# Kernel tuning notes

Hardware: AMD Instinct MI355X
Metric: run time of the kernel (lower is better)

## Reference

```python
import jax, jax.numpy as jnp
import numpy as np

FLOOR = 1e-12
B, C, T = 64, 80, 8000


def setup_inputs() -> dict:
    key = jax.random.key(0)
    k1, k2 = jax.random.split(key)
    x = jax.random.uniform(k1, (B, C, T), dtype=jnp.float32)  # nonneg energies
    x_length = jax.random.randint(k2, (B,), 1, T + 1, dtype=jnp.int32)
    # learned PCEN parameters (init values from module defaults)
    alpha = jnp.full((C,), 0.96, dtype=jnp.float32)
    delta = jnp.full((C,), 2.0, dtype=jnp.float32)
    root = jnp.full((C,), 2.0, dtype=jnp.float32)
    ema_w = jnp.full((C,), 0.04, dtype=jnp.float32)  # per-channel smooth coef (sPCEN)
    return {"x": x, "alpha": alpha, "delta": delta, "root": root,
            "ema_w": ema_w, "x_length": x_length}


def _ema(x, w):
    """Exponential moving average along time. x: (B,C,T), w: (C,). acc init = x[:,:,0]."""
    xt = jnp.moveaxis(x, 2, 0)  # (T, B, C)

    def step(acc, xi):
        acc = w * xi + (1.0 - w) * acc
        return acc, acc

    _, ys = jax.lax.scan(step, x[:, :, 0], xt)  # ys: (T, B, C)
    return jnp.moveaxis(ys, 0, 2)  # (B, C, T)


def reference(x, alpha, delta, root, ema_w, x_length):
    w = jnp.clip(ema_w, 0.0, 1.0)
    a = jnp.minimum(alpha, 1.0)[None, :, None]
    r = jnp.maximum(root, 1.0)[None, :, None]
    d = delta[None, :, None]
    m = _ema(x, w)  # (B, C, T)
    one_over_root = 1.0 / r
    out = (x / (FLOOR + m) ** a + d) ** one_over_root - d ** one_over_root
    return (out, x_length)
```

## Files before the change

kernel.cpp:

```cpp
#include <hip/hip_runtime.h>
#include <cmath>


constexpr int T_LEN = 8000;
constexpr int T4    = T_LEN / 4;
constexpr int BLK   = 256;
constexpr int NTILE = (T4 + BLK - 1) / BLK;

__device__ __forceinline__ float fexp2(float x) { return __builtin_amdgcn_exp2f(x); }
__device__ __forceinline__ float flog2(float x) { return __builtin_amdgcn_logf(x); }
__device__ __forceinline__ float fsqrt(float x) { return __builtin_amdgcn_sqrtf(x); }

__global__ __launch_bounds__(BLK, 8) void pcen_kernel(
    const float* __restrict__ x, const float* __restrict__ alpha,
    const float* __restrict__ delta, const float* __restrict__ root,
    const float* __restrict__ ema_w, const int* __restrict__ xlen,
    float* __restrict__ out, int C, int rows, int nlen)
{
    __shared__ float wB[2][4];

    const int tid  = threadIdx.x;
    const int lane = tid & 63;
    const int wid  = tid >> 6;
    const int row  = blockIdx.x;
    const int c    = row % C;

    const float w     = fminf(fmaxf(ema_w[c], 0.0f), 1.0f);
    const float p     = 1.0f - w;
    const float na    = -fminf(alpha[c], 1.0f);
    const float r     = fmaxf(root[c], 1.0f);
    const float inv_r = 1.0f / r;
    const float d     = delta[c];
    const bool  use_sqrt = (r == 2.0f);
    const float droot = use_sqrt ? fsqrt(d) : fexp2(inv_r * flog2(d));

    const float p4 = p * p * p * p;
    const float c1 = p4, c2 = c1 * c1, c3 = c2 * c2,
                c4 = c3 * c3, c5 = c4 * c4, c6 = c5 * c5;
    const float q  = c6 * c6;
    const float q2 = q * q, q3 = q2 * q, q4 = q2 * q2;
    const float lp  = flog2(p);
    const float p4l = (lane == 0) ? 1.0f : fexp2(4.0f * (float)lane * lp);
    const float qw  = (wid == 0) ? 1.0f : (wid == 1) ? q : (wid == 2) ? q2 : q3;

    const float4* x4 = reinterpret_cast<const float4*>(x + (size_t)row * T_LEN);
    float4*       o4 = reinterpret_cast<float4*>(out + (size_t)row * T_LEN);

    float carry = x[(size_t)row * T_LEN];

    float4 v = (tid < T4) ? x4[tid] : make_float4(0.f, 0.f, 0.f, 0.f);

    for (int t = 0; t < NTILE; ++t) {
        const int  j      = t * BLK + tid;
        const bool active = (j < T4);
        const int  par    = t & 1;

        float s = v.x;
        s = fmaf(s, p, v.y); s = fmaf(s, p, v.z); s = fmaf(s, p, v.w);
        float b = active ? (w * s) : 0.0f;

        float pb;
        pb = __shfl_up(b,  1, 64); if (lane >=  1) b = fmaf(c1, pb, b);
        pb = __shfl_up(b,  2, 64); if (lane >=  2) b = fmaf(c2, pb, b);
        pb = __shfl_up(b,  4, 64); if (lane >=  4) b = fmaf(c3, pb, b);
        pb = __shfl_up(b,  8, 64); if (lane >=  8) b = fmaf(c4, pb, b);
        pb = __shfl_up(b, 16, 64); if (lane >= 16) b = fmaf(c5, pb, b);
        pb = __shfl_up(b, 32, 64); if (lane >= 32) b = fmaf(c6, pb, b);

        if (lane == 63) wB[par][wid] = b;
        float eb = __shfl_up(b, 1, 64);
        if (lane == 0) eb = 0.0f;
        __syncthreads();

        float4 vn = make_float4(0.f, 0.f, 0.f, 0.f);
        const int jn = j + BLK;
        if (jn < T4) vn = x4[jn];

        const float W0 = wB[par][0], W1 = wB[par][1], W2 = wB[par][2], W3 = wB[par][3];
        float Pb = 0.0f;
        if (wid == 1) Pb = W0;
        else if (wid == 2) Pb = fmaf(q, W0, W1);
        else if (wid == 3) Pb = fmaf(q, fmaf(q, W0, W1), W2);
        const float base = fmaf(qw, carry, Pb);
        float acc = fmaf(p4l, base, eb);

        const float Tb = fmaf(q, fmaf(q, fmaf(q, W0, W1), W2), W3);
        carry = fmaf(q4, carry, Tb);

        if (active) {
            float4 u = v, o;
            if (use_sqrt) {
                acc = fmaf(w, u.x, p * acc);
                o.x = fsqrt(fmaf(u.x, fexp2(na * flog2(acc + 1e-12f)), d)) - droot;
                acc = fmaf(w, u.y, p * acc);
                o.y = fsqrt(fmaf(u.y, fexp2(na * flog2(acc + 1e-12f)), d)) - droot;
                acc = fmaf(w, u.z, p * acc);
                o.z = fsqrt(fmaf(u.z, fexp2(na * flog2(acc + 1e-12f)), d)) - droot;
                acc = fmaf(w, u.w, p * acc);
                o.w = fsqrt(fmaf(u.w, fexp2(na * flog2(acc + 1e-12f)), d)) - droot;
            } else {
                acc = fmaf(w, u.x, p * acc);
                o.x = fexp2(inv_r * flog2(fmaf(u.x, fexp2(na * flog2(acc + 1e-12f)), d))) - droot;
                acc = fmaf(w, u.y, p * acc);
                o.y = fexp2(inv_r * flog2(fmaf(u.y, fexp2(na * flog2(acc + 1e-12f)), d))) - droot;
                acc = fmaf(w, u.z, p * acc);
                o.z = fexp2(inv_r * flog2(fmaf(u.z, fexp2(na * flog2(acc + 1e-12f)), d))) - droot;
                acc = fmaf(w, u.w, p * acc);
                o.w = fexp2(inv_r * flog2(fmaf(u.w, fexp2(na * flog2(acc + 1e-12f)), d))) - droot;
            }
            o4[j] = o;
        }
        v = vn;
    }

    if (row == 0) {
        for (int i = tid; i < nlen; i += BLK)
            out[(size_t)rows * T_LEN + i] = (float)xlen[i];
    }
}

extern "C" void kernel_launch(void* const* d_in, const int* in_sizes, int n_in,
                              void* d_out, int out_size, void* d_ws, size_t ws_size,
                              hipStream_t stream) {
    const float* x     = (const float*)d_in[0];
    const float* alpha = (const float*)d_in[1];
    const float* delta = (const float*)d_in[2];
    const float* root  = (const float*)d_in[3];
    const float* emaw  = (const float*)d_in[4];
    const int*   xlen  = (const int*)d_in[5];
    float*       out   = (float*)d_out;

    const int C    = in_sizes[1];
    const int rows = in_sizes[0] / T_LEN;
    const int nlen = in_sizes[5];

    hipLaunchKernelGGL(pcen_kernel, dim3(rows), dim3(BLK), 0, stream,
                       x, alpha, delta, root, emaw, xlen, out, C, rows, nlen);
}
```

Measured before the change: 65.84 us.

## Assign one wavefront per row to eliminate block-level barrier in EMA scan

Each 64-lane wavefront now processes a whole row on its own, so the cross-wave combine through shared memory and the __syncthreads per tile are gone. The carry between tiles is passed with a lane-63 broadcast shuffle. The cost is a serial loop per wave that is four times longer (32 tiles instead of 8) with less memory-level parallelism per row. The grid shrinks to 1280 blocks, which lowers per-block overhead.

```diff
diff --git a/kernel.cpp b/kernel.cpp
--- a/kernel.cpp
+++ b/kernel.cpp
@@ -5,7 +5,7 @@
 constexpr int T_LEN = 8000;
 constexpr int T4    = T_LEN / 4;
 constexpr int BLK   = 256;
-constexpr int NTILE = (T4 + BLK - 1) / BLK;
+constexpr int NT    = (T4 + 63) / 64;
 
 __device__ __forceinline__ float fexp2(float x) { return __builtin_amdgcn_exp2f(x); }
 __device__ __forceinline__ float flog2(float x) { return __builtin_amdgcn_logf(x); }
@@ -17,104 +17,92 @@
     const float* __restrict__ ema_w, const int* __restrict__ xlen,
     float* __restrict__ out, int C, int rows, int nlen)
 {
-    __shared__ float wB[2][4];
-
     const int tid  = threadIdx.x;
     const int lane = tid & 63;
     const int wid  = tid >> 6;
-    const int row  = blockIdx.x;
-    const int c    = row % C;
+    const int row  = blockIdx.x * 4 + wid;
 
-    const float w     = fminf(fmaxf(ema_w[c], 0.0f), 1.0f);
-    const float p     = 1.0f - w;
-    const float na    = -fminf(alpha[c], 1.0f);
-    const float r     = fmaxf(root[c], 1.0f);
-    const float inv_r = 1.0f / r;
-    const float d     = delta[c];
-    const bool  use_sqrt = (r == 2.0f);
-    const float droot = use_sqrt ? fsqrt(d) : fexp2(inv_r * flog2(d));
+    if (row < rows) {
+        const int c = row % C;
 
-    const float p4 = p * p * p * p;
-    const float c1 = p4, c2 = c1 * c1, c3 = c2 * c2,
-                c4 = c3 * c3, c5 = c4 * c4, c6 = c5 * c5;
-    const float q  = c6 * c6;
-    const float q2 = q * q, q3 = q2 * q, q4 = q2 * q2;
-    const float lp  = flog2(p);
-    const float p4l = (lane == 0) ? 1.0f : fexp2(4.0f * (float)lane * lp);
-    const float qw  = (wid == 0) ? 1.0f : (wid == 1) ? q : (wid == 2) ? q2 : q3;
+        const float w     = fminf(fmaxf(ema_w[c], 0.0f), 1.0f);
+        const float p     = 1.0f - w;
+        const float na    = -fminf(alpha[c], 1.0f);
+        const float r     = fmaxf(root[c], 1.0f);
+        const float inv_r = 1.0f / r;
+        const float d     = delta[c];
+        const bool  use_sqrt = (r == 2.0f);
+        const float droot = use_sqrt ? fsqrt(d) : fexp2(inv_r * flog2(d));
 
-    const float4* x4 = reinterpret_cast<const float4*>(x + (size_t)row * T_LEN);
-    float4*       o4 = reinterpret_cast<float4*>(out + (size_t)row * T_LEN);
+        const float c1 = p * p * p * p;
+        const float c2 = c1 * c1, c3 = c2 * c2, c4 = c3 * c3,
+                    c5 = c4 * c4, c6 = c5 * c5;
+        const float q  = c6 * c6;
+        const float lp  = flog2(p);
+        const float p4l = (lane == 0) ? 1.0f : fexp2(4.0f * (float)lane * lp);
 
-    float carry = x[(size_t)row * T_LEN];
+        const float4* x4 = reinterpret_cast<const float4*>(x + (size_t)row * T_LEN);
+        float4*       o4 = reinterpret_cast<float4*>(out + (size_t)row * T_LEN);
 
-    float4 v = (tid < T4) ? x4[tid] : make_float4(0.f, 0.f, 0.f, 0.f);
+        float4 v = x4[lane];
+        float carry = __shfl(v.x, 0, 64);
 
-    for (int t = 0; t < NTILE; ++t) {
-        const int  j      = t * BLK + tid;
-        const bool active = (j < T4);
-        const int  par    = t & 1;
+        for (int t = 0; t < NT; ++t) {
+            const int  j      = t * 64 + lane;
+            const bool active = (j < T4);
 
-        float s = v.x;
-        s = fmaf(s, p, v.y); s = fmaf(s, p, v.z); s = fmaf(s, p, v.w);
-        float b = active ? (w * s) : 0.0f;
+            const int jn = j + 64;
+            float4 vn = make_float4(0.f, 0.f, 0.f, 0.f);
+            if (jn < T4) vn = x4[jn];
 
-        float pb;
-        pb = __shfl_up(b,  1, 64); if (lane >=  1) b = fmaf(c1, pb, b);
-        pb = __shfl_up(b,  2, 64); if (lane >=  2) b = fmaf(c2, pb, b);
-        pb = __shfl_up(b,  4, 64); if (lane >=  4) b = fmaf(c3, pb, b);
-        pb = __shfl_up(b,  8, 64); if (lane >=  8) b = fmaf(c4, pb, b);
-        pb = __shfl_up(b, 16, 64); if (lane >= 16) b = fmaf(c5, pb, b);
-        pb = __shfl_up(b, 32, 64); if (lane >= 32) b = fmaf(c6, pb, b);
+            float s = v.x;
+            s = fmaf(s, p, v.y); s = fmaf(s, p, v.z); s = fmaf(s, p, v.w);
+            float b = active ? (w * s) : 0.0f;
 
-        if (lane == 63) wB[par][wid] = b;
-        float eb = __shfl_up(b, 1, 64);
-        if (lane == 0) eb = 0.0f;
-        __syncthreads();
+            float pb;
+            pb = __shfl_up(b,  1, 64); if (lane >=  1) b = fmaf(c1, pb, b);
+            pb = __shfl_up(b,  2, 64); if (lane >=  2) b = fmaf(c2, pb, b);
+            pb = __shfl_up(b,  4, 64); if (lane >=  4) b = fmaf(c3, pb, b);
+            pb = __shfl_up(b,  8, 64); if (lane >=  8) b = fmaf(c4, pb, b);
+            pb = __shfl_up(b, 16, 64); if (lane >= 16) b = fmaf(c5, pb, b);
+            pb = __shfl_up(b, 32, 64); if (lane >= 32) b = fmaf(c6, pb, b);
 
-        float4 vn = make_float4(0.f, 0.f, 0.f, 0.f);
-        const int jn = j + BLK;
-        if (jn < T4) vn = x4[jn];
+            float eb = __shfl_up(b, 1, 64);
+            if (lane == 0) eb = 0.0f;
+            const float tb = __shfl(b, 63, 64);
 
-        const float W0 = wB[par][0], W1 = wB[par][1], W2 = wB[par][2], W3 = wB[par][3];
-        float Pb = 0.0f;
-        if (wid == 1) Pb = W0;
-        else if (wid == 2) Pb = fmaf(q, W0, W1);
-        else if (wid == 3) Pb = fmaf(q, fmaf(q, W0, W1), W2);
-        const float base = fmaf(qw, carry, Pb);
-        float acc = fmaf(p4l, base, eb);
+            float acc = fmaf(p4l, carry, eb);
+            carry = fmaf(q, carry, tb);
 
-        const float Tb = fmaf(q, fmaf(q, fmaf(q, W0, W1), W2), W3);
-        carry = fmaf(q4, carry, Tb);
-
-        if (active) {
-            float4 u = v, o;
-            if (use_sqrt) {
-                acc = fmaf(w, u.x, p * acc);
-                o.x = fsqrt(fmaf(u.x, fexp2(na * flog2(acc + 1e-12f)), d)) - droot;
-                acc = fmaf(w, u.y, p * acc);
-                o.y = fsqrt(fmaf(u.y, fexp2(na * flog2(acc + 1e-12f)), d)) - droot;
-                acc = fmaf(w, u.z, p * acc);
-                o.z = fsqrt(fmaf(u.z, fexp2(na * flog2(acc + 1e-12f)), d)) - droot;
-                acc = fmaf(w, u.w, p * acc);
-                o.w = fsqrt(fmaf(u.w, fexp2(na * flog2(acc + 1e-12f)), d)) - droot;
-            } else {
-                acc = fmaf(w, u.x, p * acc);
-                o.x = fexp2(inv_r * flog2(fmaf(u.x, fexp2(na * flog2(acc + 1e-12f)), d))) - droot;
-                acc = fmaf(w, u.y, p * acc);
-                o.y = fexp2(inv_r * flog2(fmaf(u.y, fexp2(na * flog2(acc + 1e-12f)), d))) - droot;
-                acc = fmaf(w, u.z, p * acc);
-                o.z = fexp2(inv_r * flog2(fmaf(u.z, fexp2(na * flog2(acc + 1e-12f)), d))) - droot;
-                acc = fmaf(w, u.w, p * acc);
-                o.w = fexp2(inv_r * flog2(fmaf(u.w, fexp2(na * flog2(acc + 1e-12f)), d))) - droot;
+            if (active) {
+                float4 u = v, o;
+                if (use_sqrt) {
+                    acc = fmaf(w, u.x, p * acc);
+                    o.x = fsqrt(fmaf(u.x, fexp2(na * flog2(acc + 1e-12f)), d)) - droot;
+                    acc = fmaf(w, u.y, p * acc);
+                    o.y = fsqrt(fmaf(u.y, fexp2(na * flog2(acc + 1e-12f)), d)) - droot;
+                    acc = fmaf(w, u.z, p * acc);
+                    o.z = fsqrt(fmaf(u.z, fexp2(na * flog2(acc + 1e-12f)), d)) - droot;
+                    acc = fmaf(w, u.w, p * acc);
+                    o.w = fsqrt(fmaf(u.w, fexp2(na * flog2(acc + 1e-12f)), d)) - droot;
+                } else {
+                    acc = fmaf(w, u.x, p * acc);
+                    o.x = fexp2(inv_r * flog2(fmaf(u.x, fexp2(na * flog2(acc + 1e-12f)), d))) - droot;
+                    acc = fmaf(w, u.y, p * acc);
+                    o.y = fexp2(inv_r * flog2(fmaf(u.y, fexp2(na * flog2(acc + 1e-12f)), d))) - droot;
+                    acc = fmaf(w, u.z, p * acc);
+                    o.z = fexp2(inv_r * flog2(fmaf(u.z, fexp2(na * flog2(acc + 1e-12f)), d))) - droot;
+                    acc = fmaf(w, u.w, p * acc);
+                    o.w = fexp2(inv_r * flog2(fmaf(u.w, fexp2(na * flog2(acc + 1e-12f)), d))) - droot;
+                }
+                o4[j] = o;
             }
-            o4[j] = o;
+            v = vn;
         }
-        v = vn;
     }
 
-    if (row == 0) {
-        for (int i = tid; i < nlen; i += BLK)
+    if (blockIdx.x == 0 && wid == 0) {
+        for (int i = lane; i < nlen; i += 64)
             out[(size_t)rows * T_LEN + i] = (float)xlen[i];
     }
 }
@@ -134,6 +122,7 @@
     const int rows = in_sizes[0] / T_LEN;
     const int nlen = in_sizes[5];
 
-    hipLaunchKernelGGL(pcen_kernel, dim3(rows), dim3(BLK), 0, stream,
+    const int nblk = (rows + 3) / 4;
+    hipLaunchKernelGGL(pcen_kernel, dim3(nblk), dim3(BLK), 0, stream,
                        x, alpha, delta, root, emaw, xlen, out, C, rows, nlen);
 }
```

Result: slower. 70.99 us (+7.8%).

## Process two float4 chunks per thread per tile to halve block barriers

Applied to the files above, without the earlier changes.

Each tile now covers 512 float4 (two per thread), so the scan runs interleaved low/high wave scans and chains two carries per tile. This cuts the number of __syncthreads and serial tile iterations per row from 8 to 4, and the next tile's loads are now issued before the scan rather than after the barrier. In exchange it uses more registers, so launch bounds drop from 8 to 6 waves-per-EU hints, which may lower occupancy.

```diff
diff --git a/kernel.cpp b/kernel.cpp
--- a/kernel.cpp
+++ b/kernel.cpp
@@ -5,19 +5,20 @@
 constexpr int T_LEN = 8000;
 constexpr int T4    = T_LEN / 4;
 constexpr int BLK   = 256;
-constexpr int NTILE = (T4 + BLK - 1) / BLK;
+constexpr int TILE4 = BLK * 2;
+constexpr int NTILE = (T4 + TILE4 - 1) / TILE4;
 
 __device__ __forceinline__ float fexp2(float x) { return __builtin_amdgcn_exp2f(x); }
 __device__ __forceinline__ float flog2(float x) { return __builtin_amdgcn_logf(x); }
 __device__ __forceinline__ float fsqrt(float x) { return __builtin_amdgcn_sqrtf(x); }
 
-__global__ __launch_bounds__(BLK, 8) void pcen_kernel(
+__global__ __launch_bounds__(BLK, 6) void pcen_kernel(
     const float* __restrict__ x, const float* __restrict__ alpha,
     const float* __restrict__ delta, const float* __restrict__ root,
     const float* __restrict__ ema_w, const int* __restrict__ xlen,
     float* __restrict__ out, int C, int rows, int nlen)
 {
-    __shared__ float wB[2][4];
+    __shared__ float wLo[2][4], wHi[2][4];
 
     const int tid  = threadIdx.x;
     const int lane = tid & 63;
@@ -34,11 +35,12 @@
     const bool  use_sqrt = (r == 2.0f);
     const float droot = use_sqrt ? fsqrt(d) : fexp2(inv_r * flog2(d));
 
-    const float p4 = p * p * p * p;
-    const float c1 = p4, c2 = c1 * c1, c3 = c2 * c2,
-                c4 = c3 * c3, c5 = c4 * c4, c6 = c5 * c5;
+    const float c1 = p * p * p * p;
+    const float c2 = c1 * c1, c3 = c2 * c2, c4 = c3 * c3,
+                c5 = c4 * c4, c6 = c5 * c5;
     const float q  = c6 * c6;
-    const float q2 = q * q, q3 = q2 * q, q4 = q2 * q2;
+    const float q2 = q * q, q3 = q2 * q;
+    const float ql = q2 * q2;
     const float lp  = flog2(p);
     const float p4l = (lane == 0) ? 1.0f : fexp2(4.0f * (float)lane * lp);
     const float qw  = (wid == 0) ? 1.0f : (wid == 1) ? q : (wid == 2) ? q2 : q3;
@@ -48,69 +50,117 @@
 
     float carry = x[(size_t)row * T_LEN];
 
-    float4 v = (tid < T4) ? x4[tid] : make_float4(0.f, 0.f, 0.f, 0.f);
+    float4 v0 = x4[tid];
+    float4 v1 = x4[tid + BLK];
 
     for (int t = 0; t < NTILE; ++t) {
-        const int  j      = t * BLK + tid;
-        const bool active = (j < T4);
+        const int  j0     = t * TILE4 + tid;
+        const int  j1     = j0 + BLK;
+        const bool hi_act = (j1 < T4);
         const int  par    = t & 1;
 
-        float s = v.x;
-        s = fmaf(s, p, v.y); s = fmaf(s, p, v.z); s = fmaf(s, p, v.w);
-        float b = active ? (w * s) : 0.0f;
+        float4 n0 = make_float4(0.f, 0.f, 0.f, 0.f);
+        float4 n1 = make_float4(0.f, 0.f, 0.f, 0.f);
+        const int k0 = j0 + TILE4, k1 = j1 + TILE4;
+        if (t + 1 < NTILE) {
+            n0 = x4[k0];
+            if (k1 < T4) n1 = x4[k1];
+        }
 
-        float pb;
-        pb = __shfl_up(b,  1, 64); if (lane >=  1) b = fmaf(c1, pb, b);
-        pb = __shfl_up(b,  2, 64); if (lane >=  2) b = fmaf(c2, pb, b);
-        pb = __shfl_up(b,  4, 64); if (lane >=  4) b = fmaf(c3, pb, b);
-        pb = __shfl_up(b,  8, 64); if (lane >=  8) b = fmaf(c4, pb, b);
-        pb = __shfl_up(b, 16, 64); if (lane >= 16) b = fmaf(c5, pb, b);
-        pb = __shfl_up(b, 32, 64); if (lane >= 32) b = fmaf(c6, pb, b);
+        float sl = v0.x;
+        sl = fmaf(sl, p, v0.y); sl = fmaf(sl, p, v0.z); sl = fmaf(sl, p, v0.w);
+        float bl = w * sl;
+        float sh = v1.x;
+        sh = fmaf(sh, p, v1.y); sh = fmaf(sh, p, v1.z); sh = fmaf(sh, p, v1.w);
+        float bh = hi_act ? (w * sh) : 0.0f;
 
-        if (lane == 63) wB[par][wid] = b;
-        float eb = __shfl_up(b, 1, 64);
-        if (lane == 0) eb = 0.0f;
+        float pl, ph;
+        pl = __shfl_up(bl,  1, 64); ph = __shfl_up(bh,  1, 64);
+        if (lane >=  1) { bl = fmaf(c1, pl, bl); bh = fmaf(c1, ph, bh); }
+        pl = __shfl_up(bl,  2, 64); ph = __shfl_up(bh,  2, 64);
+        if (lane >=  2) { bl = fmaf(c2, pl, bl); bh = fmaf(c2, ph, bh); }
+        pl = __shfl_up(bl,  4, 64); ph = __shfl_up(bh,  4, 64);
+        if (lane >=  4) { bl = fmaf(c3, pl, bl); bh = fmaf(c3, ph, bh); }
+        pl = __shfl_up(bl,  8, 64); ph = __shfl_up(bh,  8, 64);
+        if (lane >=  8) { bl = fmaf(c4, pl, bl); bh = fmaf(c4, ph, bh); }
+        pl = __shfl_up(bl, 16, 64); ph = __shfl_up(bh, 16, 64);
+        if (lane >= 16) { bl = fmaf(c5, pl, bl); bh = fmaf(c5, ph, bh); }
+        pl = __shfl_up(bl, 32, 64); ph = __shfl_up(bh, 32, 64);
+        if (lane >= 32) { bl = fmaf(c6, pl, bl); bh = fmaf(c6, ph, bh); }
+
+        if (lane == 63) { wLo[par][wid] = bl; wHi[par][wid] = bh; }
+        float ebl = __shfl_up(bl, 1, 64);
+        float ebh = __shfl_up(bh, 1, 64);
+        if (lane == 0) { ebl = 0.0f; ebh = 0.0f; }
         __syncthreads();
 
-        float4 vn = make_float4(0.f, 0.f, 0.f, 0.f);
-        const int jn = j + BLK;
-        if (jn < T4) vn = x4[jn];
+        const float L0 = wLo[par][0], L1 = wLo[par][1], L2 = wLo[par][2], L3 = wLo[par][3];
+        const float H0 = wHi[par][0], H1 = wHi[par][1], H2 = wHi[par][2], H3 = wHi[par][3];
+        float PL = 0.0f, PH = 0.0f;
+        if (wid == 1)      { PL = L0;                        PH = H0; }
+        else if (wid == 2) { PL = fmaf(q, L0, L1);           PH = fmaf(q, H0, H1); }
+        else if (wid == 3) { PL = fmaf(q, fmaf(q, L0, L1), L2);
+                             PH = fmaf(q, fmaf(q, H0, H1), H2); }
+        const float TloB = fmaf(q, fmaf(q, fmaf(q, L0, L1), L2), L3);
+        const float ThiB = fmaf(q, fmaf(q, fmaf(q, H0, H1), H2), H3);
 
-        const float W0 = wB[par][0], W1 = wB[par][1], W2 = wB[par][2], W3 = wB[par][3];
-        float Pb = 0.0f;
-        if (wid == 1) Pb = W0;
-        else if (wid == 2) Pb = fmaf(q, W0, W1);
-        else if (wid == 3) Pb = fmaf(q, fmaf(q, W0, W1), W2);
-        const float base = fmaf(qw, carry, Pb);
-        float acc = fmaf(p4l, base, eb);
+        const float Elo = fmaf(qw, carry, PL);
+        const float mid = fmaf(ql, carry, TloB);
+        const float Ehi = fmaf(qw, mid, PH);
+        carry = fmaf(ql, mid, ThiB);
 
-        const float Tb = fmaf(q, fmaf(q, fmaf(q, W0, W1), W2), W3);
-        carry = fmaf(q4, carry, Tb);
+        float accl = fmaf(p4l, Elo, ebl);
+        float acch = fmaf(p4l, Ehi, ebh);
 
-        if (active) {
-            float4 u = v, o;
+        {
+            float4 u = v0, o;
             if (use_sqrt) {
-                acc = fmaf(w, u.x, p * acc);
-                o.x = fsqrt(fmaf(u.x, fexp2(na * flog2(acc + 1e-12f)), d)) - droot;
-                acc = fmaf(w, u.y, p * acc);
-                o.y = fsqrt(fmaf(u.y, fexp2(na * flog2(acc + 1e-12f)), d)) - droot;
-                acc = fmaf(w, u.z, p * acc);
-                o.z = fsqrt(fmaf(u.z, fexp2(na * flog2(acc + 1e-12f)), d)) - droot;
-                acc = fmaf(w, u.w, p * acc);
-                o.w = fsqrt(fmaf(u.w, fexp2(na * flog2(acc + 1e-12f)), d)) - droot;
+                accl = fmaf(w, u.x, p * accl);
+                o.x = fsqrt(fmaf(u.x, fexp2(na * flog2(accl + 1e-12f)), d)) - droot;
+                accl = fmaf(w, u.y, p * accl);
+                o.y = fsqrt(fmaf(u.y, fexp2(na * flog2(accl + 1e-12f)), d)) - droot;
+                accl = fmaf(w, u.z, p * accl);
+                o.z = fsqrt(fmaf(u.z, fexp2(na * flog2(accl + 1e-12f)), d)) - droot;
+                accl = fmaf(w, u.w, p * accl);
+                o.w = fsqrt(fmaf(u.w, fexp2(na * flog2(accl + 1e-12f)), d)) - droot;
             } else {
-                acc = fmaf(w, u.x, p * acc);
-                o.x = fexp2(inv_r * flog2(fmaf(u.x, fexp2(na * flog2(acc + 1e-12f)), d))) - droot;
-                acc = fmaf(w, u.y, p * acc);
-                o.y = fexp2(inv_r * flog2(fmaf(u.y, fexp2(na * flog2(acc + 1e-12f)), d))) - droot;
-                acc = fmaf(w, u.z, p * acc);
-                o.z = fexp2(inv_r * flog2(fmaf(u.z, fexp2(na * flog2(acc + 1e-12f)), d))) - droot;
-                acc = fmaf(w, u.w, p * acc);
-                o.w = fexp2(inv_r * flog2(fmaf(u.w, fexp2(na * flog2(acc + 1e-12f)), d))) - droot;
+                accl = fmaf(w, u.x, p * accl);
+                o.x = fexp2(inv_r * flog2(fmaf(u.x, fexp2(na * flog2(accl + 1e-12f)), d))) - droot;
+                accl = fmaf(w, u.y, p * accl);
+                o.y = fexp2(inv_r * flog2(fmaf(u.y, fexp2(na * flog2(accl + 1e-12f)), d))) - droot;
+                accl = fmaf(w, u.z, p * accl);
+                o.z = fexp2(inv_r * flog2(fmaf(u.z, fexp2(na * flog2(accl + 1e-12f)), d))) - droot;
+                accl = fmaf(w, u.w, p * accl);
+                o.w = fexp2(inv_r * flog2(fmaf(u.w, fexp2(na * flog2(accl + 1e-12f)), d))) - droot;
             }
-            o4[j] = o;
+            o4[j0] = o;
         }
-        v = vn;
+        if (hi_act) {
+            float4 u = v1, o;
+            if (use_sqrt) {
+                acch = fmaf(w, u.x, p * acch);
+                o.x = fsqrt(fmaf(u.x, fexp2(na * flog2(acch + 1e-12f)), d)) - droot;
+                acch = fmaf(w, u.y, p * acch);
+                o.y = fsqrt(fmaf(u.y, fexp2(na * flog2(acch + 1e-12f)), d)) - droot;
+                acch = fmaf(w, u.z, p * acch);
+                o.z = fsqrt(fmaf(u.z, fexp2(na * flog2(acch + 1e-12f)), d)) - droot;
+                acch = fmaf(w, u.w, p * acch);
+                o.w = fsqrt(fmaf(u.w, fexp2(na * flog2(acch + 1e-12f)), d)) - droot;
+            } else {
+                acch = fmaf(w, u.x, p * acch);
+                o.x = fexp2(inv_r * flog2(fmaf(u.x, fexp2(na * flog2(acch + 1e-12f)), d))) - droot;
+                acch = fmaf(w, u.y, p * acch);
+                o.y = fexp2(inv_r * flog2(fmaf(u.y, fexp2(na * flog2(acch + 1e-12f)), d))) - droot;
+                acch = fmaf(w, u.z, p * acch);
+                o.z = fexp2(inv_r * flog2(fmaf(u.z, fexp2(na * flog2(acch + 1e-12f)), d))) - droot;
+                acch = fmaf(w, u.w, p * acch);
+                o.w = fexp2(inv_r * flog2(fmaf(u.w, fexp2(na * flog2(acch + 1e-12f)), d))) - droot;
+            }
+            o4[j1] = o;
+        }
+
+        v0 = n0;
+        v1 = n1;
     }
 
     if (row == 0) {
```

Measured after the change: 64.71 us. Within noise of the previous version (-1.7%).

## Load whole row into registers and batch scans with single barrier

Applied to the files above, without the earlier changes.

Each block now loads all 8 float4 tiles of its row up front, runs the eight intra-wave shuffle scans interleaved, and syncs once instead of once per tile. The carry is then chained across tiles serially. Output uses nontemporal stores, and the launch-bounds occupancy hint drops from 8 to 6 to make room for the extra registers. This gives more loads in flight and more independent shuffles at the cost of higher register pressure and lower occupancy.

```diff
diff --git a/kernel.cpp b/kernel.cpp
--- a/kernel.cpp
+++ b/kernel.cpp
@@ -5,19 +5,26 @@
 constexpr int T_LEN = 8000;
 constexpr int T4    = T_LEN / 4;
 constexpr int BLK   = 256;
-constexpr int NTILE = (T4 + BLK - 1) / BLK;
+constexpr int NH    = 8;
+
+typedef float f32x4 __attribute__((ext_vector_type(4)));
 
 __device__ __forceinline__ float fexp2(float x) { return __builtin_amdgcn_exp2f(x); }
 __device__ __forceinline__ float flog2(float x) { return __builtin_amdgcn_logf(x); }
 __device__ __forceinline__ float fsqrt(float x) { return __builtin_amdgcn_sqrtf(x); }
 
-__global__ __launch_bounds__(BLK, 8) void pcen_kernel(
+__device__ __forceinline__ void nt_store4(float* dst, float a, float b, float c, float d) {
+    f32x4 v = { a, b, c, d };
+    __builtin_nontemporal_store(v, reinterpret_cast<f32x4*>(dst));
+}
+
+__global__ __launch_bounds__(BLK, 6) void pcen_kernel(
     const float* __restrict__ x, const float* __restrict__ alpha,
     const float* __restrict__ delta, const float* __restrict__ root,
     const float* __restrict__ ema_w, const int* __restrict__ xlen,
     float* __restrict__ out, int C, int rows, int nlen)
 {
-    __shared__ float wB[2][4];
+    __shared__ float wS[NH][4];
 
     const int tid  = threadIdx.x;
     const int lane = tid & 63;
@@ -34,83 +41,98 @@
     const bool  use_sqrt = (r == 2.0f);
     const float droot = use_sqrt ? fsqrt(d) : fexp2(inv_r * flog2(d));
 
-    const float p4 = p * p * p * p;
-    const float c1 = p4, c2 = c1 * c1, c3 = c2 * c2,
-                c4 = c3 * c3, c5 = c4 * c4, c6 = c5 * c5;
+    const float c1 = p * p * p * p;
+    const float c2 = c1 * c1, c3 = c2 * c2, c4 = c3 * c3,
+                c5 = c4 * c4, c6 = c5 * c5;
     const float q  = c6 * c6;
-    const float q2 = q * q, q3 = q2 * q, q4 = q2 * q2;
+    const float q2 = q * q, q3 = q2 * q;
+    const float ql = q2 * q2;
     const float lp  = flog2(p);
     const float p4l = (lane == 0) ? 1.0f : fexp2(4.0f * (float)lane * lp);
     const float qw  = (wid == 0) ? 1.0f : (wid == 1) ? q : (wid == 2) ? q2 : q3;
 
-    const float4* x4 = reinterpret_cast<const float4*>(x + (size_t)row * T_LEN);
-    float4*       o4 = reinterpret_cast<float4*>(out + (size_t)row * T_LEN);
+    const float4* x4   = reinterpret_cast<const float4*>(x + (size_t)row * T_LEN);
+    float*        orow = out + (size_t)row * T_LEN;
 
+    float4 v[NH];
+    #pragma unroll
+    for (int h = 0; h < NH; ++h) {
+        const int j = h * BLK + tid;
+        if (j < T4) v[h] = x4[j];
+        else        v[h] = make_float4(0.f, 0.f, 0.f, 0.f);
+    }
     float carry = x[(size_t)row * T_LEN];
 
-    float4 v = (tid < T4) ? x4[tid] : make_float4(0.f, 0.f, 0.f, 0.f);
+    float b[NH];
+    #pragma unroll
+    for (int h = 0; h < NH; ++h) {
+        float s = v[h].x;
+        s = fmaf(s, p, v[h].y); s = fmaf(s, p, v[h].z); s = fmaf(s, p, v[h].w);
+        b[h] = w * s;
+    }
 
-    for (int t = 0; t < NTILE; ++t) {
-        const int  j      = t * BLK + tid;
-        const bool active = (j < T4);
-        const int  par    = t & 1;
+    {
+        float pb;
+        #pragma unroll
+        for (int h = 0; h < NH; ++h) { pb = __shfl_up(b[h],  1, 64); if (lane >=  1) b[h] = fmaf(c1, pb, b[h]); }
+        #pragma unroll
+        for (int h = 0; h < NH; ++h) { pb = __shfl_up(b[h],  2, 64); if (lane >=  2) b[h] = fmaf(c2, pb, b[h]); }
+        #pragma unroll
+        for (int h = 0; h < NH; ++h) { pb = __shfl_up(b[h],  4, 64); if (lane >=  4) b[h] = fmaf(c3, pb, b[h]); }
+        #pragma unroll
+        for (int h = 0; h < NH; ++h) { pb = __shfl_up(b[h],  8, 64); if (lane >=  8) b[h] = fmaf(c4, pb, b[h]); }
+        #pragma unroll
+        for (int h = 0; h < NH; ++h) { pb = __shfl_up(b[h], 16, 64); if (lane >= 16) b[h] = fmaf(c5, pb, b[h]); }
+        #pragma unroll
+        for (int h = 0; h < NH; ++h) { pb = __shfl_up(b[h], 32, 64); if (lane >= 32) b[h] = fmaf(c6, pb, b[h]); }
+    }
 
-        float s = v.x;
-        s = fmaf(s, p, v.y); s = fmaf(s, p, v.z); s = fmaf(s, p, v.w);
-        float b = active ? (w * s) : 0.0f;
+    float eb[NH];
+    #pragma unroll
+    for (int h = 0; h < NH; ++h) {
+        if (lane == 63) wS[h][wid] = b[h];
+        eb[h] = __shfl_up(b[h], 1, 64);
+        if (lane == 0) eb[h] = 0.0f;
+    }
+    __syncthreads();
 
-        float pb;
-        pb = __shfl_up(b,  1, 64); if (lane >=  1) b = fmaf(c1, pb, b);
-        pb = __shfl_up(b,  2, 64); if (lane >=  2) b = fmaf(c2, pb, b);
-        pb = __shfl_up(b,  4, 64); if (lane >=  4) b = fmaf(c3, pb, b);
-        pb = __shfl_up(b,  8, 64); if (lane >=  8) b = fmaf(c4, pb, b);
-        pb = __shfl_up(b, 16, 64); if (lane >= 16) b = fmaf(c5, pb, b);
-        pb = __shfl_up(b, 32, 64); if (lane >= 32) b = fmaf(c6, pb, b);
+    #pragma unroll
+    for (int h = 0; h < NH; ++h) {
+        const float W0 = wS[h][0], W1 = wS[h][1], W2 = wS[h][2], W3 = wS[h][3];
+        float P = 0.0f;
+        if (wid == 1)      P = W0;
+        else if (wid == 2) P = fmaf(q, W0, W1);
+        else if (wid == 3) P = fmaf(q, fmaf(q, W0, W1), W2);
+        const float E  = fmaf(qw, carry, P);
+        const float Tb = fmaf(q, fmaf(q, fmaf(q, W0, W1), W2), W3);
+        carry = fmaf(ql, carry, Tb);
 
-        if (lane == 63) wB[par][wid] = b;
-        float eb = __shfl_up(b, 1, 64);
-        if (lane == 0) eb = 0.0f;
-        __syncthreads();
-
-        float4 vn = make_float4(0.f, 0.f, 0.f, 0.f);
-        const int jn = j + BLK;
-        if (jn < T4) vn = x4[jn];
-
-        const float W0 = wB[par][0], W1 = wB[par][1], W2 = wB[par][2], W3 = wB[par][3];
-        float Pb = 0.0f;
-        if (wid == 1) Pb = W0;
-        else if (wid == 2) Pb = fmaf(q, W0, W1);
-        else if (wid == 3) Pb = fmaf(q, fmaf(q, W0, W1), W2);
-        const float base = fmaf(qw, carry, Pb);
-        float acc = fmaf(p4l, base, eb);
-
-        const float Tb = fmaf(q, fmaf(q, fmaf(q, W0, W1), W2), W3);
-        carry = fmaf(q4, carry, Tb);
-
-        if (active) {
-            float4 u = v, o;
+        const int j = h * BLK + tid;
+        if (j < T4) {
+            float acc = fmaf(p4l, E, eb[h]);
+            const float4 u = v[h];
+            float ox, oy, oz, ow;
             if (use_sqrt) {
                 acc = fmaf(w, u.x, p * acc);
-                o.x = fsqrt(fmaf(u.x, fexp2(na * flog2(acc + 1e-12f)), d)) - droot;
+                ox = fsqrt(fmaf(u.x, fexp2(na * flog2(acc + 1e-12f)), d)) - droot;
                 acc = fmaf(w, u.y, p * acc);
-                o.y = fsqrt(fmaf(u.y, fexp2(na * flog2(acc + 1e-12f)), d)) - droot;
+                oy = fsqrt(fmaf(u.y, fexp2(na * flog2(acc + 1e-12f)), d)) - droot;
                 acc = fmaf(w, u.z, p * acc);
-                o.z = fsqrt(fmaf(u.z, fexp2(na * flog2(acc + 1e-12f)), d)) - droot;
+                oz = fsqrt(fmaf(u.z, fexp2(na * flog2(acc + 1e-12f)), d)) - droot;
                 acc = fmaf(w, u.w, p * acc);
-                o.w = fsqrt(fmaf(u.w, fexp2(na * flog2(acc + 1e-12f)), d)) - droot;
+                ow = fsqrt(fmaf(u.w, fexp2(na * flog2(acc + 1e-12f)), d)) - droot;
             } else {
                 acc = fmaf(w, u.x, p * acc);
-                o.x = fexp2(inv_r * flog2(fmaf(u.x, fexp2(na * flog2(acc + 1e-12f)), d))) - droot;
+                ox = fexp2(inv_r * flog2(fmaf(u.x, fexp2(na * flog2(acc + 1e-12f)), d))) - droot;
                 acc = fmaf(w, u.y, p * acc);
-                o.y = fexp2(inv_r * flog2(fmaf(u.y, fexp2(na * flog2(acc + 1e-12f)), d))) - droot;
+                oy = fexp2(inv_r * flog2(fmaf(u.y, fexp2(na * flog2(acc + 1e-12f)), d))) - droot;
                 acc = fmaf(w, u.z, p * acc);
-                o.z = fexp2(inv_r * flog2(fmaf(u.z, fexp2(na * flog2(acc + 1e-12f)), d))) - droot;
+                oz = fexp2(inv_r * flog2(fmaf(u.z, fexp2(na * flog2(acc + 1e-12f)), d))) - droot;
                 acc = fmaf(w, u.w, p * acc);
-                o.w = fexp2(inv_r * flog2(fmaf(u.w, fexp2(na * flog2(acc + 1e-12f)), d))) - droot;
+                ow = fexp2(inv_r * flog2(fmaf(u.w, fexp2(na * flog2(acc + 1e-12f)), d))) - droot;
             }
-            o4[j] = o;
+            nt_store4(orow + (size_t)j * 4, ox, oy, oz, ow);
         }
-        v = vn;
     }
 
     if (row == 0) {
```

Measured after the change: 57.31 us. 1.15x faster.
